# Optimization experiments

Hardware: AMD Instinct MI355X
Metric: run time of the kernel (lower is better)

## Reference

```python
import jax, jax.numpy as jnp
import numpy as np

B, CIN, H, W = 4, 256, 128, 128
PL = 128                     # plane == width (base_width=32, groups=1)
K, PAD, STR, DIL = 3, 1, 1, 1
KK = K * K


def setup_inputs() -> dict:
    key = jax.random.key(0)
    ks = jax.random.split(key, 24)
    rn = lambda k, s, sc=1.0: jax.random.normal(k, s, jnp.float32) * sc
    un = lambda k, s: jax.random.uniform(k, s, jnp.float32, 0.5, 1.5)
    return {
        'x': rn(ks[0], (B, CIN, H, W)),
        # conv1 (1x1, bias=False) + its folded eval-mode BN (scale/shift), then the extra bn1
        'w1': rn(ks[1], (PL, CIN), 0.05),
        's1a': un(ks[2], (PL,)), 't1a': rn(ks[3], (PL,), 0.1),
        's1b': un(ks[4], (PL,)), 't1b': rn(ks[5], (PL,), 0.1),
        # ModulatedDeformConvPack: offset/mask conv (3*K*K out channels) + deform conv weight/bias
        'w_off': rn(ks[6], (3 * KK, PL, K, K), 0.01),
        'b_off': rn(ks[7], (3 * KK,), 0.01),
        'w_dc': rn(ks[8], (PL, PL, K, K), 0.05),
        'b_dc': rn(ks[9], (PL,), 0.05),
        's2': un(ks[10], (PL,)), 't2': rn(ks[11], (PL,), 0.1),
        # conv3 (1x1, bias=False) + folded BN, then extra bn3
        'w3': rn(ks[12], (PL, PL), 0.05),
        's3a': un(ks[13], (PL,)), 't3a': rn(ks[14], (PL,), 0.1),
        's3b': un(ks[15], (PL,)), 't3b': rn(ks[16], (PL,), 0.1),
        # downsample: 1x1 conv (default bias=True) + folded BN
        'w_ds': rn(ks[17], (PL, CIN), 0.05),
        'b_ds': rn(ks[18], (PL,), 0.05),
        'sd': un(ks[19], (PL,)), 'td': rn(ks[20], (PL,), 0.1),
    }


def bn(x, s, t):
    # eval-mode BatchNorm folded to per-channel affine
    return x * s[None, :, None, None] + t[None, :, None, None]


def conv1x1(x, w):
    return jnp.einsum('bchw,oc->bohw', x, w)


def conv3x3(x, w, b):
    y = jax.lax.conv_general_dilated(
        x, w, (STR, STR), [(PAD, PAD), (PAD, PAD)], rhs_dilation=(DIL, DIL),
        dimension_numbers=('NCHW', 'OIHW', 'NCHW'))
    return y + b[None, :, None, None]


def bilinear_sample(x, py, px):
    """x: [B,C,H,W]; py/px: [B,KK,Ho,Wo] absolute sampling coords.
    Zero padding outside the image (per-corner validity, as in DCNv2)."""
    Bx, C, Hx, Wx = x.shape
    y0 = jnp.floor(py)
    x0 = jnp.floor(px)
    wy = py - y0   # [B,KK,Ho,Wo]
    wx = px - x0
    y0i = y0.astype(jnp.int32)
    x0i = x0.astype(jnp.int32)

    def per_b(xb, y0b, x0b, wyb, wxb):
        xf = xb.reshape(C, Hx * Wx)
        def g(iy, ix):
            valid = ((iy >= 0) & (iy < Hx) & (ix >= 0) & (ix < Wx)).astype(xb.dtype)
            idx = (jnp.clip(iy, 0, Hx - 1) * Wx + jnp.clip(ix, 0, Wx - 1)).reshape(-1)
            return jnp.take(xf, idx, axis=1).reshape((C,) + iy.shape) * valid[None]
        v00 = g(y0b, x0b)
        v01 = g(y0b, x0b + 1)
        v10 = g(y0b + 1, x0b)
        v11 = g(y0b + 1, x0b + 1)
        return (v00 * ((1 - wyb) * (1 - wxb))[None] + v01 * ((1 - wyb) * wxb)[None]
              + v10 * (wyb * (1 - wxb))[None] + v11 * (wyb * wxb)[None])

    return jax.vmap(per_b)(x, y0i, x0i, wy, wx)   # [B,C,KK,Ho,Wo]


def reference(x, w1, s1a, t1a, s1b, t1b, w_off, b_off, w_dc, b_dc, s2, t2,
              w3, s3a, t3a, s3b, t3b, w_ds, b_ds, sd, td):
    # conv1 sequential (conv+BN+ReLU), then the redundant bn1+relu from forward()
    out = jax.nn.relu(bn(conv1x1(x, w1), s1a, t1a))
    out = jax.nn.relu(bn(out, s1b, t1b))

    # --- ModulatedDeformConvPack (DCNv2) ---
    off = conv3x3(out, w_off, b_off)              # [B,3*KK,Ho,Wo]
    o1, o2, o3 = jnp.split(off, 3, axis=1)        # dy, dx, mask logits: each [B,KK,Ho,Wo]
    mask = jax.nn.sigmoid(o3)
    Ho, Wo = o1.shape[2], o1.shape[3]
    ky = (jnp.repeat(jnp.arange(K), K) * DIL).astype(jnp.float32)   # [KK]
    kx = (jnp.tile(jnp.arange(K), K) * DIL).astype(jnp.float32)
    base_y = (jnp.arange(Ho) * STR - PAD).astype(jnp.float32)
    base_x = (jnp.arange(Wo) * STR - PAD).astype(jnp.float32)
    py = base_y[None, None, :, None] + ky[None, :, None, None] + o1  # [B,KK,Ho,Wo]
    px = base_x[None, None, None, :] + kx[None, :, None, None] + o2
    sampled = bilinear_sample(out, py, px) * mask[:, None]           # [B,C,KK,Ho,Wo]
    out = jnp.einsum('oik,bikhw->bohw', w_dc.reshape(PL, PL, KK), sampled)
    out = out + b_dc[None, :, None, None]

    out = jax.nn.relu(bn(out, s2, t2))            # bn2 + relu
    out = jax.nn.relu(bn(conv1x1(out, w3), s3a, t3a))   # conv3 sequential
    out = bn(out, s3b, t3b)                       # bn3

    ident = bn(conv1x1(x, w_ds) + b_ds[None, :, None, None], sd, td)  # downsample
    return jax.nn.relu(out + ident)
```

## Files before the change

kernel.cpp:

```cpp
#include <hip/hip_runtime.h>
#include <hip/hip_bf16.h>
#include <hip/hip_fp16.h>

#define HW 16384

typedef unsigned short u16;
typedef unsigned int   u32;
typedef __attribute__((ext_vector_type(8))) short short8v;
typedef __attribute__((ext_vector_type(8))) _Float16 half8v;
typedef __attribute__((ext_vector_type(2))) __fp16 fp16x2;
typedef __attribute__((ext_vector_type(4))) float float4v;

__device__ __forceinline__ float b2f(u16 v) { return __uint_as_float((u32)v << 16); }
__device__ __forceinline__ u16 f2bf(float f) {
  u32 u = __float_as_uint(f);
  u32 r = (u + 0x7fffu + ((u >> 16) & 1u)) >> 16;
  return (u16)r;
}
__device__ __forceinline__ u16 f2h(float f) {
  _Float16 h = (_Float16)f;
  return *(u16*)&h;
}
__device__ __forceinline__ float bflo(u32 u) { return __uint_as_float(u << 16); }
__device__ __forceinline__ float bfhi(u32 u) { return __uint_as_float(u & 0xffff0000u); }
__device__ __forceinline__ u32 pkt(float a, float b) {
  return __builtin_amdgcn_perm(__float_as_uint(b), __float_as_uint(a), 0x07060302u);
}
__device__ __forceinline__ u16 bft(float v) { return (u16)(__float_as_uint(v) >> 16); }
__device__ __forceinline__ u32 pkh(float a, float b) {
  union { fp16x2 h; u32 u; } cv;
  cv.h = __builtin_amdgcn_cvt_pkrtz(a, b);
  return cv.u;
}

__global__ __launch_bounds__(256) void k_init(const float* __restrict__ w_dc,
                                              const float* __restrict__ w1,
                                              const float* __restrict__ w_ds,
                                              const float* __restrict__ w3,
                                              const float* __restrict__ w_off,
                                              u16* __restrict__ wTb, u16* __restrict__ wB1,
                                              u16* __restrict__ w3b, u16* __restrict__ woffb) {
  int idx = blockIdx.x * 256 + threadIdx.x;
  if (idx < 147456) {
    int ntile = idx / 18432, r = idx % 18432;
    int ks = r / 512, r2 = r % 512;
    int lane = r2 / 8, j = r2 % 8;
    int o = ntile * 16 + (lane & 15);
    int k = ks * 32 + ((lane >> 4) * 8) + j;
    int tap = k >> 7, ci = k & 127;
    wTb[idx] = f2h(w_dc[(o * 128 + ci) * 9 + tap]);
  }
  int i1 = idx - 147456;
  if (i1 >= 0 && i1 < 65536) {
    int ntile = i1 / 4096, r = i1 % 4096;
    int ks = r / 512, r2 = r % 512;
    int lane = r2 / 8, j = r2 % 8;
    int o = ntile * 16 + (lane & 15);
    int c = ks * 32 + ((lane >> 4) * 8) + j;
    float v = (ntile < 8) ? w1[o * 256 + c] : w_ds[(o - 128) * 256 + c];
    wB1[i1] = f2bf(v);
  }
  int i2 = idx - 212992;
  if (i2 >= 0 && i2 < 16384) {
    int ntile = i2 / 2048, r = i2 % 2048;
    int ks = r / 512, r2 = r % 512;
    int lane = r2 / 8, j = r2 % 8;
    int o = ntile * 16 + (lane & 15);
    int c = ks * 32 + ((lane >> 4) * 8) + j;
    w3b[i2] = f2bf(w3[o * 128 + c]);
  }
  int i3 = idx - 229376;
  if (i3 >= 0 && i3 < 36864) {
    int ntile = i3 / 18432, r = i3 % 18432;
    int ks = r / 512, r2 = r % 512;
    int lane = r2 / 8, j = r2 % 8;
    int oc = ntile * 16 + (lane & 15);
    int k = ks * 32 + ((lane >> 4) * 8) + j;
    int tap = k >> 7, c = k & 127;
    woffb[i3] = (oc < 27) ? f2h(w_off[oc * 1152 + c * 9 + tap]) : (u16)0;
  }
}

__global__ __launch_bounds__(256) void k_fused1(const float* __restrict__ x,
                                                const u16* __restrict__ wB1,
                                                const float* __restrict__ s1a, const float* __restrict__ t1a,
                                                const float* __restrict__ s1b, const float* __restrict__ t1b,
                                                const float* __restrict__ b_ds,
                                                const float* __restrict__ sd, const float* __restrict__ td,
                                                u16* __restrict__ out1,
                                                u16* __restrict__ identb)
{
  __shared__ __align__(16) u16 xA[8704];
  const int tid = threadIdx.x;
  const int wq = blockIdx.x, h = blockIdx.y, b = blockIdx.z;
  const int wave = tid >> 6, lane = tid & 63;

  {
    const float* xb = x + (size_t)b * 256 * HW + h * 128 + wq * 32;
    u32* dst = (u32*)xA;
    int cp = tid >> 3, wg = tid & 7;
#pragma unroll
    for (int i = 0; i < 4; ++i) {
      int cpair = i * 32 + cp;
      int c0 = cpair * 2;
      float4 va = *(const float4*)&xb[(size_t)c0 * HW + wg * 4];
      float4 vb = *(const float4*)&xb[(size_t)(c0 + 1) * HW + wg * 4];
      int p0 = wg * 4;
      dst[(p0 + 0) * 133 + cpair] = pkt(va.x, vb.x);
      dst[(p0 + 1) * 133 + cpair] = pkt(va.y, vb.y);
      dst[(p0 + 2) * 133 + cpair] = pkt(va.z, vb.z);
      dst[(p0 + 3) * 133 + cpair] = pkt(va.w, vb.w);
    }
  }
  __syncthreads();

  const int nlo = lane & 15, kgr = lane >> 4;
  float4v acc[2][4];
#pragma unroll
  for (int mt = 0; mt < 2; ++mt)
#pragma unroll
    for (int nt = 0; nt < 4; ++nt) acc[mt][nt] = (float4v)(0.f);

  const u16* a0p = &xA[nlo * 266 + kgr * 8];
  const u16* a1p = &xA[(nlo + 16) * 266 + kgr * 8];
  const u16* bp = &wB1[(((size_t)(wave * 4) * 8) * 64 + lane) * 8];

#pragma unroll
  for (int ks = 0; ks < 8; ++ks) {
    short8v a0 = *(const short8v*)(a0p + ks * 32);
    short8v a1 = *(const short8v*)(a1p + ks * 32);
#pragma unroll
    for (int nt = 0; nt < 4; ++nt) {
      short8v bv = *(const short8v*)(bp + nt * 4096 + ks * 512);
      acc[0][nt] = __builtin_amdgcn_mfma_f32_16x16x32_bf16(a0, bv, acc[0][nt], 0, 0, 0);
      acc[1][nt] = __builtin_amdgcn_mfma_f32_16x16x32_bf16(a1, bv, acc[1][nt], 0, 0, 0);
    }
  }
  __syncthreads();

  u16* P1 = xA;
  u16* T1 = xA + 4352;

  const int rbase = kgr * 4;
  if (wave < 2) {
#pragma unroll
    for (int nt = 0; nt < 4; ++nt) {
      int o = (wave * 4 + nt) * 16 + nlo;
      float sa = s1a[o], ta = t1a[o], sb = s1b[o], tb = t1b[o];
#pragma unroll
      for (int mt = 0; mt < 2; ++mt)
#pragma unroll
        for (int r = 0; r < 4; ++r) {
          float v = acc[mt][nt][r];
          v = fmaxf(sa * v + ta, 0.f);
          v = fmaxf(sb * v + tb, 0.f);
          int pos = mt * 16 + rbase + r;
          P1[pos * 136 + o] = f2h(v);
        }
    }
  } else {
#pragma unroll
    for (int nt = 0; nt < 4; ++nt) {
      int og = (wave * 4 + nt) * 16 + nlo - 128;
      float sv = sd[og], tv = td[og], bv = b_ds[og];
#pragma unroll
      for (int mt = 0; mt < 2; ++mt)
#pragma unroll
        for (int r = 0; r < 4; ++r) {
          float v = sv * (acc[mt][nt][r] + bv) + tv;
          T1[og * 34 + mt * 16 + rbase + r] = bft(v);
        }
    }
  }
  __syncthreads();

  {
    size_t rowbase = ((size_t)((b * 128 + h) * 128 + wq * 32)) * 128;
#pragma unroll
    for (int i = 0; i < 2; ++i) {
      int s = i * 256 + tid;
      int pos = s >> 4, q = s & 15;
      uint4 v = *(const uint4*)&P1[pos * 136 + q * 8];
      *(uint4*)&out1[rowbase + (size_t)pos * 128 + q * 8] = v;
    }
  }
  {
    int o = tid >> 1, half = tid & 1;
    const u16* src = &T1[o * 34 + half * 16];
    u32 bb[8];
#pragma unroll
    for (int i = 0; i < 8; ++i) bb[i] = *(const u32*)(src + i * 2);
    size_t g = ((size_t)((b * 128 + o) * 128 + h)) * 128 + wq * 32 + half * 16;
    *(uint4*)&identb[g] = make_uint4(bb[0], bb[1], bb[2], bb[3]);
    *(uint4*)&identb[g + 8] = make_uint4(bb[4], bb[5], bb[6], bb[7]);
  }
}

__global__ __launch_bounds__(512) void k_dcn(const u16* __restrict__ out1,
                                             const u16* __restrict__ wTb,
                                             const u16* __restrict__ w3b,
                                             const u16* __restrict__ woffb,
                                             const float* __restrict__ b_off,
                                             const float* __restrict__ b_dc,
                                             const float* __restrict__ s2, const float* __restrict__ t2,
                                             const float* __restrict__ s3a, const float* __restrict__ t3a,
                                             const float* __restrict__ s3b, const float* __restrict__ t3b,
                                             const u16* __restrict__ identb,
                                             float* __restrict__ out) {
  __shared__ __align__(16) u16 U[25024];

  u16*   W    = U;
  u32*   Jl   = (u32*)((char*)U + 32640);
  float* offp = (float*)((char*)U + 41856);
  float* Pp   = (float*)((char*)U + 9216);
  u16*   P    = U;
  float* T2   = (float*)((char*)U + 9216);

  const int tid = threadIdx.x;
  const int flat = blockIdx.x + (blockIdx.y << 3) + (blockIdx.z << 9);
  const int nid = (flat & 7) * 256 + (flat >> 3);
  const int wq = nid & 7, h2 = (nid >> 3) & 63, b = nid >> 9;
  const int h = h2 * 2;
  const int wave = tid >> 6, lane = tid & 63;
  const int nlo = lane & 15, kgr = lane >> 4;
  const u16* base = out1 + (size_t)b * HW * 128;
  const int w0 = wq * 16;

  for (int k = tid; k < 1920; k += 512) {
    int pix = k >> 4, q = k & 15;
    int ri = pix / 20, ci = pix % 20;
    int y = h - 2 + ri, x = w0 - 2 + ci;
    uint4 g = make_uint4(0u, 0u, 0u, 0u);
    if ((y >= 0) & (y < 128) & (x >= 0) & (x < 128))
      g = *(const uint4*)&base[((size_t)(y * 128 + x)) * 128 + q * 8];
    *(uint4*)&W[pix * 136 + q * 8] = g;
  }
  __syncthreads();

  {
    const int ntile = wave & 1, mt = (wave >> 1) & 1, kg = wave >> 2;
    const int t0 = kg ? 5 : 0, t1 = kg ? 9 : 5;
    float4v oacc = (float4v)(0.f);
    for (int t = t0; t < t1; ++t) {
      int ty = t / 3, tx = t % 3;
      const u16* bp = &woffb[(((size_t)(ntile * 36 + t * 4)) * 64 + lane) * 8];
      const u16* ap = &W[((mt + ty + 1) * 20 + nlo + tx + 1) * 136 + kgr * 8];
#pragma unroll
      for (int ksl = 0; ksl < 4; ++ksl) {
        half8v bv = *(const half8v*)(bp + ksl * 512);
        half8v a = *(const half8v*)(ap + ksl * 32);
        oacc = __builtin_amdgcn_mfma_f32_16x16x32_f16(a, bv, oacc, 0, 0, 0);
      }
    }
    int oc = ntile * 16 + nlo;
#pragma unroll
    for (int r = 0; r < 4; ++r)
      offp[kg * 1024 + (mt * 16 + kgr * 4 + r) * 32 + oc] = oacc[r];
  }
  __syncthreads();

  if (tid < 288) {
    int pos = tid / 9, tap = tid % 9;
    int pr = pos >> 4, pc = pos & 15;
    int hh = h + pr, w = w0 + pc;
    float dy  = offp[pos * 32 + tap]      + offp[1024 + pos * 32 + tap]      + b_off[tap];
    float dxv = offp[pos * 32 + 9 + tap]  + offp[1024 + pos * 32 + 9 + tap]  + b_off[9 + tap];
    float sg  = offp[pos * 32 + 18 + tap] + offp[1024 + pos * 32 + 18 + tap] + b_off[18 + tap];
    float mk = 1.f / (1.f + __expf(-sg));
    float py = (float)(hh - 1 + tap / 3) + dy;
    float px = (float)(w - 1 + tap % 3) + dxv;
    float fy = floorf(py), fx = floorf(px);
    int y0 = (int)fy, x0 = (int)fx;
    float wy = py - fy, wxf = px - fx;
    bool vy0 = (y0 >= 0) & (y0 < 128), vy1 = (y0 >= -1) & (y0 < 127);
    bool vx0 = (x0 >= 0) & (x0 < 128), vx1 = (x0 >= -1) & (x0 < 127);
    float w00 = (vy0 & vx0) ? (1.f - wy) * (1.f - wxf) * mk : 0.f;
    float w01 = (vy0 & vx1) ? (1.f - wy) * wxf * mk : 0.f;
    float w10 = (vy1 & vx0) ? wy * (1.f - wxf) * mk : 0.f;
    float w11 = (vy1 & vx1) ? wy * wxf * mk : 0.f;
    int y0c = min(max(y0, 0), 127), y1c = min(max(y0 + 1, 0), 127);
    int x0c = min(max(x0, 0), 127), x1c = min(max(x0 + 1, 0), 127);
    auto enc = [&](int yc, int xc) -> u32 {
      int ri = yc - (h - 2), ci = xc - (w0 - 2);
      if (((unsigned)ri < 6u) && ((unsigned)ci < 20u))
        return 0x80000000u | (u32)((ri * 20 + ci) * 136);
      return (u32)((yc * 128 + xc) * 128);
    };
    u32* jt = &Jl[tid * 8];
    jt[0] = enc(y0c, x0c);
    jt[1] = enc(y0c, x1c);
    jt[2] = enc(y1c, x0c);
    jt[3] = enc(y1c, x1c);
    ((float*)jt)[4] = w00; ((float*)jt)[5] = w01;
    ((float*)jt)[6] = w10; ((float*)jt)[7] = w11;
  }
  __syncthreads();

  float4v acc8[8];
#pragma unroll
  for (int nt = 0; nt < 8; ++nt) acc8[nt] = (float4v)(0.f);
  {
    const int ks = wave & 3, mh = wave >> 2;
    const int ch0 = ks * 32 + kgr * 8;
    const int jrow = (mh * 16 + nlo) * 9;

#pragma unroll
    for (int t = 0; t < 9; ++t) {
      const u32* jt = &Jl[(jrow + t) * 8];
      uint4 co4 = *(const uint4*)jt;
      float4 w4 = *(const float4*)(jt + 4);
      u32 cos[4] = {co4.x, co4.y, co4.z, co4.w};
      float wf[4] = {w4.x, w4.y, w4.z, w4.w};
      float alo[4] = {0.f, 0.f, 0.f, 0.f};
      float ahi[4] = {0.f, 0.f, 0.f, 0.f};
#pragma unroll
      for (int c = 0; c < 4; ++c) {
        u32 co = cos[c];
        short8v cv;
        if (co & 0x80000000u)
          cv = *(const short8v*)&W[(co & 0x7fffffffu) + ch0];
        else
          cv = *(const short8v*)(base + co + ch0);
        union { short8v s; _Float16 h[8]; } cc; cc.s = cv;
        float wk = wf[c];
#pragma unroll
        for (int p = 0; p < 4; ++p) {
          alo[p] = fmaf(wk, (float)cc.h[2 * p],     alo[p]);
          ahi[p] = fmaf(wk, (float)cc.h[2 * p + 1], ahi[p]);
        }
      }
      union { u32 u[4]; half8v s; } av;
#pragma unroll
      for (int p = 0; p < 4; ++p) av.u[p] = pkh(alo[p], ahi[p]);
      {
        const u16* bb = &wTb[(((size_t)(t * 4 + ks)) * 64 + lane) * 8];
        __builtin_amdgcn_s_setprio(1);
#pragma unroll
        for (int nt = 0; nt < 8; ++nt) {
          half8v bv = *(const half8v*)(bb + (size_t)nt * 18432);
          acc8[nt] = __builtin_amdgcn_mfma_f32_16x16x32_f16(av.s, bv, acc8[nt], 0, 0, 0);
        }
        __builtin_amdgcn_s_setprio(0);
      }
    }
  }
  __syncthreads();

  {
    const int ks = wave & 3, mh = wave >> 2;
    if (kgr < 2) {
#pragma unroll
      for (int nt = 0; nt < 8; ++nt)
#pragma unroll
        for (int r = 0; r < 4; ++r)
          Pp[mh * 4096 + ks * 1024 + (kgr * 4 + r) * 128 + nt * 16 + nlo] = acc8[nt][r];
    }
    __syncthreads();
#pragma unroll
    for (int q = 0; q < 4; ++q) {
      int idx = q * 512 + tid;
      int mi = idx >> 10, rem = idx & 1023;
      int p8 = rem >> 7, o = rem & 127;
      const float* Pb = Pp + mi * 4096 + p8 * 128 + o;
      float s = Pb[0] + Pb[1024] + Pb[2048] + Pb[3072];
      float v = s + b_dc[o];
      v = fmaxf(s2[o] * v + t2[o], 0.f);
      P[(mi * 16 + p8) * 136 + o] = bft(v);
    }
    __syncthreads();
    if (kgr >= 2) {
#pragma unroll
      for (int nt = 0; nt < 8; ++nt)
#pragma unroll
        for (int r = 0; r < 4; ++r)
          Pp[mh * 4096 + ks * 1024 + ((kgr - 2) * 4 + r) * 128 + nt * 16 + nlo] = acc8[nt][r];
    }
    __syncthreads();
#pragma unroll
    for (int q = 0; q < 4; ++q) {
      int idx = q * 512 + tid;
      int mi = idx >> 10, rem = idx & 1023;
      int p8 = rem >> 7, o = rem & 127;
      const float* Pb = Pp + mi * 4096 + p8 * 128 + o;
      float s = Pb[0] + Pb[1024] + Pb[2048] + Pb[3072];
      float v = s + b_dc[o];
      v = fmaxf(s2[o] * v + t2[o], 0.f);
      P[(mi * 16 + 8 + p8) * 136 + o] = bft(v);
    }
    __syncthreads();
  }

  float4v acc2[2];
  acc2[0] = (float4v)(0.f); acc2[1] = (float4v)(0.f);
  {
    const u16* bp3 = &w3b[(((size_t)(wave * 4)) * 64 + lane) * 8];
#pragma unroll
    for (int ks3 = 0; ks3 < 4; ++ks3) {
      short8v bv = *(const short8v*)(bp3 + ks3 * 512);
#pragma unroll
      for (int mt = 0; mt < 2; ++mt) {
        short8v a = *(const short8v*)&P[(mt * 16 + nlo) * 136 + ks3 * 32 + kgr * 8];
        acc2[mt] = __builtin_amdgcn_mfma_f32_16x16x32_bf16(a, bv, acc2[mt], 0, 0, 0);
      }
    }
  }

  {
    int o = wave * 16 + nlo;
    float sa = s3a[o], ta = t3a[o], sb = s3b[o], tb = t3b[o];
#pragma unroll
    for (int mt = 0; mt < 2; ++mt)
#pragma unroll
      for (int r = 0; r < 4; ++r) {
        float v = acc2[mt][r];
        v = fmaxf(sa * v + ta, 0.f);
        v = sb * v + tb;
        T2[o * 33 + mt * 16 + kgr * 4 + r] = v;
      }
  }
  __syncthreads();

  {
    int o = tid >> 2, qd = tid & 3;
    size_t g = ((size_t)((b * 128 + o) * 128 + h + (qd >> 1))) * 128 + w0 + (qd & 1) * 8;
    const float* trow = &T2[o * 33 + qd * 8];
    uint4 iv = *(const uint4*)&identb[g];
    u32 iw[4] = {iv.x, iv.y, iv.z, iv.w};
    float4 ov[2];
#pragma unroll
    for (int q = 0; q < 2; ++q) {
      float r0 = trow[q * 4 + 0] + bflo(iw[q * 2]);
      float r1 = trow[q * 4 + 1] + bfhi(iw[q * 2]);
      float r2 = trow[q * 4 + 2] + bflo(iw[q * 2 + 1]);
      float r3 = trow[q * 4 + 3] + bfhi(iw[q * 2 + 1]);
      ov[q] = make_float4(fmaxf(r0, 0.f), fmaxf(r1, 0.f), fmaxf(r2, 0.f), fmaxf(r3, 0.f));
    }
    *(float4*)&out[g] = ov[0];
    *(float4*)&out[g + 4] = ov[1];
  }
}

extern "C" void kernel_launch(void* const* d_in, const int* in_sizes, int n_in,
                              void* d_out, int out_size, void* d_ws, size_t ws_size,
                              hipStream_t stream) {
  const float* x     = (const float*)d_in[0];
  const float* w1    = (const float*)d_in[1];
  const float* s1a   = (const float*)d_in[2];
  const float* t1a   = (const float*)d_in[3];
  const float* s1b   = (const float*)d_in[4];
  const float* t1b   = (const float*)d_in[5];
  const float* w_off = (const float*)d_in[6];
  const float* b_off = (const float*)d_in[7];
  const float* w_dc  = (const float*)d_in[8];
  const float* b_dc  = (const float*)d_in[9];
  const float* s2    = (const float*)d_in[10];
  const float* t2    = (const float*)d_in[11];
  const float* w3    = (const float*)d_in[12];
  const float* s3a   = (const float*)d_in[13];
  const float* t3a   = (const float*)d_in[14];
  const float* s3b   = (const float*)d_in[15];
  const float* t3b   = (const float*)d_in[16];
  const float* w_ds  = (const float*)d_in[17];
  const float* b_ds  = (const float*)d_in[18];
  const float* sd    = (const float*)d_in[19];
  const float* td    = (const float*)d_in[20];

  char* ws = (char*)d_ws;
  u16* wTb    = (u16*)(ws + 0);
  u16* wB1    = (u16*)(ws + 294912);
  u16* w3b    = (u16*)(ws + 425984);
  u16* woffb  = (u16*)(ws + 458752);
  u16* out1   = (u16*)(ws + 532480);
  u16* identb = (u16*)(ws + 17309696);

  k_init  <<<1040, 256, 0, stream>>>(w_dc, w1, w_ds, w3, w_off, wTb, wB1, w3b, woffb);
  k_fused1<<<dim3(4, 128, 4), 256, 0, stream>>>(x, wB1, s1a, t1a, s1b, t1b, b_ds, sd, td, out1, identb);
  k_dcn   <<<dim3(8, 64, 4), 512, 0, stream>>>(out1, wTb, w3b, woffb, b_off, b_dc, s2, t2,
                                               s3a, t3a, s3b, t3b, identb, (float*)d_out);
}
```

Baseline: 240.4 us.

## Enlarge DCN block tile to 4x16 pixels, reusing weight fragments across two M-tiles

Each k_dcn block now covers 4 rows by 16 columns instead of 2 rows, which halves the grid. Every wave builds two sampled A fragments and applies each loaded w_dc B fragment to both, so weight loads and the halo load are amortized over twice as many pixels. The offset conv drops its K-split across waves, and the bilinear table entries are computed into registers before being written over the offset buffer. The cost is a larger LDS footprint, about 73KB, plus more accumulators (64 floats) per thread. That may lower occupancy or cause spills despite the launch_bounds hint.

```diff
diff --git a/kernel.cpp b/kernel.cpp
--- a/kernel.cpp
+++ b/kernel.cpp
@@ -196,40 +196,39 @@
   }
 }
 
-__global__ __launch_bounds__(512) void k_dcn(const u16* __restrict__ out1,
-                                             const u16* __restrict__ wTb,
-                                             const u16* __restrict__ w3b,
-                                             const u16* __restrict__ woffb,
-                                             const float* __restrict__ b_off,
-                                             const float* __restrict__ b_dc,
-                                             const float* __restrict__ s2, const float* __restrict__ t2,
-                                             const float* __restrict__ s3a, const float* __restrict__ t3a,
-                                             const float* __restrict__ s3b, const float* __restrict__ t3b,
-                                             const u16* __restrict__ identb,
-                                             float* __restrict__ out) {
-  __shared__ __align__(16) u16 U[25024];
+__global__ __launch_bounds__(512, 4) void k_dcn(const u16* __restrict__ out1,
+                                                const u16* __restrict__ wTb,
+                                                const u16* __restrict__ w3b,
+                                                const u16* __restrict__ woffb,
+                                                const float* __restrict__ b_off,
+                                                const float* __restrict__ b_dc,
+                                                const float* __restrict__ s2, const float* __restrict__ t2,
+                                                const float* __restrict__ s3a, const float* __restrict__ t3a,
+                                                const float* __restrict__ s3b, const float* __restrict__ t3b,
+                                                const u16* __restrict__ identb,
+                                                float* __restrict__ out) {
+  __shared__ __align__(16) u16 U[36416];
 
   u16*   W    = U;
-  u32*   Jl   = (u32*)((char*)U + 32640);
-  float* offp = (float*)((char*)U + 41856);
-  float* Pp   = (float*)((char*)U + 9216);
+  float* offp = (float*)((char*)U + 54400);
+  u32*   Jl   = (u32*)((char*)U + 54400);
+  float* Pp   = (float*)((char*)U + 17408);
   u16*   P    = U;
-  float* T2   = (float*)((char*)U + 9216);
+  float* T2   = (float*)((char*)U + 17408);
 
   const int tid = threadIdx.x;
-  const int flat = blockIdx.x + (blockIdx.y << 3) + (blockIdx.z << 9);
-  const int nid = (flat & 7) * 256 + (flat >> 3);
-  const int wq = nid & 7, h2 = (nid >> 3) & 63, b = nid >> 9;
-  const int h = h2 * 2;
+  const int flat = blockIdx.x + (blockIdx.y << 3) + (blockIdx.z << 8);
+  const int nid = (flat & 7) * 128 + (flat >> 3);
+  const int wq = nid & 7, th = (nid >> 3) & 31, b = nid >> 8;
+  const int h0 = th * 4, w0 = wq * 16;
   const int wave = tid >> 6, lane = tid & 63;
   const int nlo = lane & 15, kgr = lane >> 4;
   const u16* base = out1 + (size_t)b * HW * 128;
-  const int w0 = wq * 16;
-
-  for (int k = tid; k < 1920; k += 512) {
+
+  for (int k = tid; k < 3200; k += 512) {
     int pix = k >> 4, q = k & 15;
     int ri = pix / 20, ci = pix % 20;
-    int y = h - 2 + ri, x = w0 - 2 + ci;
+    int y = h0 - 2 + ri, x = w0 - 2 + ci;
     uint4 g = make_uint4(0u, 0u, 0u, 0u);
     if ((y >= 0) & (y < 128) & (x >= 0) & (x < 128))
       g = *(const uint4*)&base[((size_t)(y * 128 + x)) * 128 + q * 8];
@@ -238,10 +237,9 @@
   __syncthreads();
 
   {
-    const int ntile = wave & 1, mt = (wave >> 1) & 1, kg = wave >> 2;
-    const int t0 = kg ? 5 : 0, t1 = kg ? 9 : 5;
+    const int ntile = wave & 1, mt = wave >> 1;
     float4v oacc = (float4v)(0.f);
-    for (int t = t0; t < t1; ++t) {
+    for (int t = 0; t < 9; ++t) {
       int ty = t / 3, tx = t % 3;
       const u16* bp = &woffb[(((size_t)(ntile * 36 + t * 4)) * 64 + lane) * 8];
       const u16* ap = &W[((mt + ty + 1) * 20 + nlo + tx + 1) * 136 + kgr * 8];
@@ -255,58 +253,74 @@
     int oc = ntile * 16 + nlo;
 #pragma unroll
     for (int r = 0; r < 4; ++r)
-      offp[kg * 1024 + (mt * 16 + kgr * 4 + r) * 32 + oc] = oacc[r];
-  }
-  __syncthreads();
-
-  if (tid < 288) {
-    int pos = tid / 9, tap = tid % 9;
-    int pr = pos >> 4, pc = pos & 15;
-    int hh = h + pr, w = w0 + pc;
-    float dy  = offp[pos * 32 + tap]      + offp[1024 + pos * 32 + tap]      + b_off[tap];
-    float dxv = offp[pos * 32 + 9 + tap]  + offp[1024 + pos * 32 + 9 + tap]  + b_off[9 + tap];
-    float sg  = offp[pos * 32 + 18 + tap] + offp[1024 + pos * 32 + 18 + tap] + b_off[18 + tap];
-    float mk = 1.f / (1.f + __expf(-sg));
-    float py = (float)(hh - 1 + tap / 3) + dy;
-    float px = (float)(w - 1 + tap % 3) + dxv;
-    float fy = floorf(py), fx = floorf(px);
-    int y0 = (int)fy, x0 = (int)fx;
-    float wy = py - fy, wxf = px - fx;
-    bool vy0 = (y0 >= 0) & (y0 < 128), vy1 = (y0 >= -1) & (y0 < 127);
-    bool vx0 = (x0 >= 0) & (x0 < 128), vx1 = (x0 >= -1) & (x0 < 127);
-    float w00 = (vy0 & vx0) ? (1.f - wy) * (1.f - wxf) * mk : 0.f;
-    float w01 = (vy0 & vx1) ? (1.f - wy) * wxf * mk : 0.f;
-    float w10 = (vy1 & vx0) ? wy * (1.f - wxf) * mk : 0.f;
-    float w11 = (vy1 & vx1) ? wy * wxf * mk : 0.f;
-    int y0c = min(max(y0, 0), 127), y1c = min(max(y0 + 1, 0), 127);
-    int x0c = min(max(x0, 0), 127), x1c = min(max(x0 + 1, 0), 127);
-    auto enc = [&](int yc, int xc) -> u32 {
-      int ri = yc - (h - 2), ci = xc - (w0 - 2);
-      if (((unsigned)ri < 6u) && ((unsigned)ci < 20u))
-        return 0x80000000u | (u32)((ri * 20 + ci) * 136);
-      return (u32)((yc * 128 + xc) * 128);
-    };
-    u32* jt = &Jl[tid * 8];
-    jt[0] = enc(y0c, x0c);
-    jt[1] = enc(y0c, x1c);
-    jt[2] = enc(y1c, x0c);
-    jt[3] = enc(y1c, x1c);
-    ((float*)jt)[4] = w00; ((float*)jt)[5] = w01;
-    ((float*)jt)[6] = w10; ((float*)jt)[7] = w11;
-  }
-  __syncthreads();
-
-  float4v acc8[8];
-#pragma unroll
-  for (int nt = 0; nt < 8; ++nt) acc8[nt] = (float4v)(0.f);
+      offp[(mt * 16 + kgr * 4 + r) * 32 + oc] = oacc[r];
+  }
+  __syncthreads();
+
+  u32  jc[2][4];
+  float jw[2][4];
+#pragma unroll
+  for (int it = 0; it < 2; ++it) {
+    int j = tid + it * 512;
+    if (j < 576) {
+      int pos = j / 9, tap = j % 9;
+      int pr = pos >> 4, pc = pos & 15;
+      int hh = h0 + pr, w = w0 + pc;
+      float dy  = offp[pos * 32 + tap]      + b_off[tap];
+      float dxv = offp[pos * 32 + 9 + tap]  + b_off[9 + tap];
+      float sg  = offp[pos * 32 + 18 + tap] + b_off[18 + tap];
+      float mk = 1.f / (1.f + __expf(-sg));
+      float py = (float)(hh - 1 + tap / 3) + dy;
+      float px = (float)(w - 1 + tap % 3) + dxv;
+      float fy = floorf(py), fx = floorf(px);
+      int y0 = (int)fy, x0 = (int)fx;
+      float wy = py - fy, wxf = px - fx;
+      bool vy0 = (y0 >= 0) & (y0 < 128), vy1 = (y0 >= -1) & (y0 < 127);
+      bool vx0 = (x0 >= 0) & (x0 < 128), vx1 = (x0 >= -1) & (x0 < 127);
+      jw[it][0] = (vy0 & vx0) ? (1.f - wy) * (1.f - wxf) * mk : 0.f;
+      jw[it][1] = (vy0 & vx1) ? (1.f - wy) * wxf * mk : 0.f;
+      jw[it][2] = (vy1 & vx0) ? wy * (1.f - wxf) * mk : 0.f;
+      jw[it][3] = (vy1 & vx1) ? wy * wxf * mk : 0.f;
+      int y0c = min(max(y0, 0), 127), y1c = min(max(y0 + 1, 0), 127);
+      int x0c = min(max(x0, 0), 127), x1c = min(max(x0 + 1, 0), 127);
+      auto enc = [&](int yc, int xc) -> u32 {
+        int ri = yc - (h0 - 2), ci = xc - (w0 - 2);
+        if (((unsigned)ri < 10u) && ((unsigned)ci < 20u))
+          return 0x80000000u | (u32)((ri * 20 + ci) * 136);
+        return (u32)((yc * 128 + xc) * 128);
+      };
+      jc[it][0] = enc(y0c, x0c);
+      jc[it][1] = enc(y0c, x1c);
+      jc[it][2] = enc(y1c, x0c);
+      jc[it][3] = enc(y1c, x1c);
+    }
+  }
+  __syncthreads();
+#pragma unroll
+  for (int it = 0; it < 2; ++it) {
+    int j = tid + it * 512;
+    if (j < 576) {
+      u32* jt = &Jl[j * 8];
+      jt[0] = jc[it][0]; jt[1] = jc[it][1]; jt[2] = jc[it][2]; jt[3] = jc[it][3];
+      ((float*)jt)[4] = jw[it][0]; ((float*)jt)[5] = jw[it][1];
+      ((float*)jt)[6] = jw[it][2]; ((float*)jt)[7] = jw[it][3];
+    }
+  }
+  __syncthreads();
+
+  float4v acc8[2][8];
+#pragma unroll
+  for (int ms = 0; ms < 2; ++ms)
+#pragma unroll
+    for (int nt = 0; nt < 8; ++nt) acc8[ms][nt] = (float4v)(0.f);
   {
     const int ks = wave & 3, mh = wave >> 2;
     const int ch0 = ks * 32 + kgr * 8;
-    const int jrow = (mh * 16 + nlo) * 9;
-
-#pragma unroll
-    for (int t = 0; t < 9; ++t) {
-      const u32* jt = &Jl[(jrow + t) * 8];
+    const int jrowA = (mh * 32 + nlo) * 9;
+    const int jrowB = jrowA + 144;
+
+    auto BLD = [&](int jidx) -> half8v {
+      const u32* jt = &Jl[jidx * 8];
       uint4 co4 = *(const uint4*)jt;
       float4 w4 = *(const float4*)(jt + 4);
       u32 cos[4] = {co4.x, co4.y, co4.z, co4.w};
@@ -332,73 +346,63 @@
       union { u32 u[4]; half8v s; } av;
 #pragma unroll
       for (int p = 0; p < 4; ++p) av.u[p] = pkh(alo[p], ahi[p]);
-      {
-        const u16* bb = &wTb[(((size_t)(t * 4 + ks)) * 64 + lane) * 8];
-        __builtin_amdgcn_s_setprio(1);
-#pragma unroll
-        for (int nt = 0; nt < 8; ++nt) {
-          half8v bv = *(const half8v*)(bb + (size_t)nt * 18432);
-          acc8[nt] = __builtin_amdgcn_mfma_f32_16x16x32_f16(av.s, bv, acc8[nt], 0, 0, 0);
-        }
-        __builtin_amdgcn_s_setprio(0);
-      }
+      return av.s;
+    };
+
+#pragma unroll
+    for (int t = 0; t < 9; ++t) {
+      half8v av0 = BLD(jrowA + t);
+      half8v av1 = BLD(jrowB + t);
+      const u16* bb = &wTb[(((size_t)(t * 4 + ks)) * 64 + lane) * 8];
+      __builtin_amdgcn_s_setprio(1);
+#pragma unroll
+      for (int nt = 0; nt < 8; ++nt) {
+        half8v bv = *(const half8v*)(bb + (size_t)nt * 18432);
+        acc8[0][nt] = __builtin_amdgcn_mfma_f32_16x16x32_f16(av0, bv, acc8[0][nt], 0, 0, 0);
+        acc8[1][nt] = __builtin_amdgcn_mfma_f32_16x16x32_f16(av1, bv, acc8[1][nt], 0, 0, 0);
+      }
+      __builtin_amdgcn_s_setprio(0);
     }
   }
   __syncthreads();
 
   {
     const int ks = wave & 3, mh = wave >> 2;
-    if (kgr < 2) {
-#pragma unroll
-      for (int nt = 0; nt < 8; ++nt)
-#pragma unroll
-        for (int r = 0; r < 4; ++r)
-          Pp[mh * 4096 + ks * 1024 + (kgr * 4 + r) * 128 + nt * 16 + nlo] = acc8[nt][r];
-    }
-    __syncthreads();
-#pragma unroll
-    for (int q = 0; q < 4; ++q) {
-      int idx = q * 512 + tid;
-      int mi = idx >> 10, rem = idx & 1023;
-      int p8 = rem >> 7, o = rem & 127;
-      const float* Pb = Pp + mi * 4096 + p8 * 128 + o;
-      float s = Pb[0] + Pb[1024] + Pb[2048] + Pb[3072];
-      float v = s + b_dc[o];
-      v = fmaxf(s2[o] * v + t2[o], 0.f);
-      P[(mi * 16 + p8) * 136 + o] = bft(v);
-    }
-    __syncthreads();
-    if (kgr >= 2) {
-#pragma unroll
-      for (int nt = 0; nt < 8; ++nt)
-#pragma unroll
-        for (int r = 0; r < 4; ++r)
-          Pp[mh * 4096 + ks * 1024 + ((kgr - 2) * 4 + r) * 128 + nt * 16 + nlo] = acc8[nt][r];
-    }
-    __syncthreads();
-#pragma unroll
-    for (int q = 0; q < 4; ++q) {
-      int idx = q * 512 + tid;
-      int mi = idx >> 10, rem = idx & 1023;
-      int p8 = rem >> 7, o = rem & 127;
-      const float* Pb = Pp + mi * 4096 + p8 * 128 + o;
-      float s = Pb[0] + Pb[1024] + Pb[2048] + Pb[3072];
-      float v = s + b_dc[o];
-      v = fmaxf(s2[o] * v + t2[o], 0.f);
-      P[(mi * 16 + 8 + p8) * 136 + o] = bft(v);
-    }
-    __syncthreads();
-  }
-
-  float4v acc2[2];
-  acc2[0] = (float4v)(0.f); acc2[1] = (float4v)(0.f);
+#pragma unroll
+    for (int s = 0; s < 4; ++s) {
+      const int smh = s >> 1, sms = s & 1;
+      if (mh == smh) {
+#pragma unroll
+        for (int nt = 0; nt < 8; ++nt)
+#pragma unroll
+          for (int r = 0; r < 4; ++r)
+            Pp[ks * 2048 + (kgr * 4 + r) * 128 + nt * 16 + nlo] = acc8[sms][nt][r];
+      }
+      __syncthreads();
+#pragma unroll
+      for (int q = 0; q < 4; ++q) {
+        int idx = q * 512 + tid;
+        int p16 = idx >> 7, o = idx & 127;
+        const float* Pb = Pp + p16 * 128 + o;
+        float sum = Pb[0] + Pb[2048] + Pb[4096] + Pb[6144];
+        float v = sum + b_dc[o];
+        v = fmaxf(s2[o] * v + t2[o], 0.f);
+        P[(s * 16 + p16) * 136 + o] = bft(v);
+      }
+      __syncthreads();
+    }
+  }
+
+  float4v acc2[4];
+#pragma unroll
+  for (int mt = 0; mt < 4; ++mt) acc2[mt] = (float4v)(0.f);
   {
     const u16* bp3 = &w3b[(((size_t)(wave * 4)) * 64 + lane) * 8];
 #pragma unroll
     for (int ks3 = 0; ks3 < 4; ++ks3) {
       short8v bv = *(const short8v*)(bp3 + ks3 * 512);
 #pragma unroll
-      for (int mt = 0; mt < 2; ++mt) {
+      for (int mt = 0; mt < 4; ++mt) {
         short8v a = *(const short8v*)&P[(mt * 16 + nlo) * 136 + ks3 * 32 + kgr * 8];
         acc2[mt] = __builtin_amdgcn_mfma_f32_16x16x32_bf16(a, bv, acc2[mt], 0, 0, 0);
       }
@@ -409,34 +413,33 @@
     int o = wave * 16 + nlo;
     float sa = s3a[o], ta = t3a[o], sb = s3b[o], tb = t3b[o];
 #pragma unroll
-    for (int mt = 0; mt < 2; ++mt)
+    for (int mt = 0; mt < 4; ++mt)
 #pragma unroll
       for (int r = 0; r < 4; ++r) {
         float v = acc2[mt][r];
         v = fmaxf(sa * v + ta, 0.f);
         v = sb * v + tb;
-        T2[o * 33 + mt * 16 + kgr * 4 + r] = v;
+        T2[o * 65 + mt * 16 + kgr * 4 + r] = v;
       }
   }
   __syncthreads();
 
   {
     int o = tid >> 2, qd = tid & 3;
-    size_t g = ((size_t)((b * 128 + o) * 128 + h + (qd >> 1))) * 128 + w0 + (qd & 1) * 8;
-    const float* trow = &T2[o * 33 + qd * 8];
-    uint4 iv = *(const uint4*)&identb[g];
-    u32 iw[4] = {iv.x, iv.y, iv.z, iv.w};
-    float4 ov[2];
-#pragma unroll
-    for (int q = 0; q < 2; ++q) {
+    size_t g = ((size_t)((b * 128 + o) * 128 + h0 + qd)) * 128 + w0;
+    const float* trow = &T2[o * 65 + qd * 16];
+    uint4 iv0 = *(const uint4*)&identb[g];
+    uint4 iv1 = *(const uint4*)&identb[g + 8];
+    u32 iw[8] = {iv0.x, iv0.y, iv0.z, iv0.w, iv1.x, iv1.y, iv1.z, iv1.w};
+#pragma unroll
+    for (int q = 0; q < 4; ++q) {
       float r0 = trow[q * 4 + 0] + bflo(iw[q * 2]);
       float r1 = trow[q * 4 + 1] + bfhi(iw[q * 2]);
       float r2 = trow[q * 4 + 2] + bflo(iw[q * 2 + 1]);
       float r3 = trow[q * 4 + 3] + bfhi(iw[q * 2 + 1]);
-      ov[q] = make_float4(fmaxf(r0, 0.f), fmaxf(r1, 0.f), fmaxf(r2, 0.f), fmaxf(r3, 0.f));
-    }
-    *(float4*)&out[g] = ov[0];
-    *(float4*)&out[g + 4] = ov[1];
+      float4 ov = make_float4(fmaxf(r0, 0.f), fmaxf(r1, 0.f), fmaxf(r2, 0.f), fmaxf(r3, 0.f));
+      *(float4*)&out[g + q * 4] = ov;
+    }
   }
 }
 
@@ -475,6 +478,6 @@
 
   k_init  <<<1040, 256, 0, stream>>>(w_dc, w1, w_ds, w3, w_off, wTb, wB1, w3b, woffb);
   k_fused1<<<dim3(4, 128, 4), 256, 0, stream>>>(x, wB1, s1a, t1a, s1b, t1b, b_ds, sd, td, out1, identb);
-  k_dcn   <<<dim3(8, 64, 4), 512, 0, stream>>>(out1, wTb, w3b, woffb, b_off, b_dc, s2, t2,
+  k_dcn   <<<dim3(8, 32, 4), 512, 0, stream>>>(out1, wTb, w3b, woffb, b_off, b_dc, s2, t2,
                                                s3a, t3a, s3b, t3b, identb, (float*)d_out);
 }
```

Result: faster. 227.2 us, median of 2 (-5.5%).
